# Optimization experiments

Measured on AMD Instinct MI355X. Metric: run time of the kernel, lower is better.

The kernel has to match this reference:

```python
import jax, jax.numpy as jnp
import numpy as np

B, N, D, H, FF = 40, 257, 1024, 16, 4096
HD = D // H
SCALE = HD ** -0.5


def _layernorm(x, w, b, eps=1e-5):
    mu = jnp.mean(x, axis=-1, keepdims=True)
    var = jnp.var(x, axis=-1, keepdims=True)
    return (x - mu) * jax.lax.rsqrt(var + eps) * w + b


def _quick_gelu(x):
    return x * jax.nn.sigmoid(1.702 * x)


def setup_inputs() -> dict:
    key = jax.random.key(0)
    ks = jax.random.split(key, 8)
    s = 0.02
    return {
        'hidden_states': jax.random.normal(ks[0], (B, N, D), jnp.float32),
        'ln1_w': jnp.ones((D,), jnp.float32),
        'ln1_b': jnp.zeros((D,), jnp.float32),
        'wq': jax.random.normal(ks[1], (D, D), jnp.float32) * s,
        'bq': jnp.zeros((D,), jnp.float32),
        'wk': jax.random.normal(ks[2], (D, D), jnp.float32) * s,
        'bk': jnp.zeros((D,), jnp.float32),
        'wv': jax.random.normal(ks[3], (D, D), jnp.float32) * s,
        'bv': jnp.zeros((D,), jnp.float32),
        'wo': jax.random.normal(ks[4], (D, D), jnp.float32) * s,
        'bo': jnp.zeros((D,), jnp.float32),
        'ln2_w': jnp.ones((D,), jnp.float32),
        'ln2_b': jnp.zeros((D,), jnp.float32),
        'fc1_w': jax.random.normal(ks[5], (FF, D), jnp.float32) * s,
        'fc1_b': jnp.zeros((FF,), jnp.float32),
        'fc2_w': jax.random.normal(ks[6], (D, FF), jnp.float32) * s,
        'fc2_b': jnp.zeros((D,), jnp.float32),
    }


def reference(hidden_states, ln1_w, ln1_b, wq, bq, wk, bk, wv, bv, wo, bo,
              ln2_w, ln2_b, fc1_w, fc1_b, fc2_w, fc2_b):
    bsz, n, dim = hidden_states.shape
    residual = hidden_states
    x = _layernorm(hidden_states, ln1_w, ln1_b)
    # QKV projections (torch Linear: y = x @ W^T + b)
    q = (x @ wq.T + bq) * SCALE
    k = x @ wk.T + bk
    v = x @ wv.T + bv
    # [b, h, n, hd]
    q = q.reshape(bsz, n, H, HD).transpose(0, 2, 1, 3)
    k = k.reshape(bsz, n, H, HD).transpose(0, 2, 1, 3)
    v = v.reshape(bsz, n, H, HD).transpose(0, 2, 1, 3)
    scores = jnp.einsum('bhqd,bhkd->bhqk', q, k)  # [b,h,n,n]
    attn = jax.nn.softmax(scores, axis=-1)
    out = jnp.einsum('bhqk,bhkd->bhqd', attn, v)
    out = out.transpose(0, 2, 1, 3).reshape(bsz, n, dim)
    out = out @ wo.T + bo
    hidden = residual + out
    residual = hidden
    h2 = _layernorm(hidden, ln2_w, ln2_b)
    h2 = _quick_gelu(h2 @ fc1_w.T + fc1_b)
    h2 = h2 @ fc2_w.T + fc2_b
    return residual + h2
```

## Files before the change

### kernel.cpp

```cpp
#include <hip/hip_runtime.h>
#include <math.h>

#define D_DIM 1024
#define FF_DIM 4096
#define N_SEQ 257
#define B_SZ 40
#define H_CNT 16
#define HD_DIM 64
#define M_TOK (B_SZ * N_SEQ)
#define VT_NP 320

typedef unsigned short u16;
typedef unsigned char u8;
typedef __bf16 bf16x8 __attribute__((ext_vector_type(8)));
typedef float f32x4 __attribute__((ext_vector_type(4)));
typedef int i32x4 __attribute__((ext_vector_type(4)));

__device__ __forceinline__ float b2f(u16 u) {
    union { unsigned int i; float f; } x; x.i = ((unsigned int)u) << 16; return x.f;
}
__device__ __forceinline__ u16 f2b(float f) {
    union { float f; unsigned int i; } x; x.f = f;
    unsigned int r = x.i + 0x7FFFu + ((x.i >> 16) & 1u);
    return (u16)(r >> 16);
}
__device__ __forceinline__ unsigned q8(float f, float s) {
    int q = __float2int_rn(f * s);
    q = q < -127 ? -127 : (q > 127 ? 127 : q);
    return (unsigned)q & 0xFFu;
}

__device__ __forceinline__ void g2lds16(const void* g, void* l) {
    __builtin_amdgcn_global_load_lds(
        (const __attribute__((address_space(1))) void*)g,
        (__attribute__((address_space(3))) void*)l,
        16, 0, 0);
}

__global__ __launch_bounds__(256)
void cvt_all_kernel(const float* __restrict__ wq, const float* __restrict__ wk,
                    const float* __restrict__ wv, const float* __restrict__ wo,
                    const float* __restrict__ w1, const float* __restrict__ w2,
                    const float* __restrict__ bq, const float* __restrict__ bk,
                    const float* __restrict__ bv,
                    u16* __restrict__ wdst, u8* __restrict__ w1i8,
                    u8* __restrict__ w2i8, float* __restrict__ bqkv) {
    const int nDD = D_DIM * D_DIM, nFD = FF_DIM * D_DIM;
    const int WB8 = (4 * nDD) / 8;
    const int WF8 = (2 * nFD) / 8;
    const int tid = blockIdx.x * 256 + threadIdx.x;
    if (tid < WB8) {
        const int i = tid * 8;
        const float* src; int s;
        if (i < nDD)          { src = wq; s = i; }
        else if (i < 2 * nDD) { src = wk; s = i - nDD; }
        else if (i < 3 * nDD) { src = wv; s = i - 2 * nDD; }
        else                  { src = wo; s = i - 3 * nDD; }
        float4 a = *(const float4*)(src + s);
        float4 b = *(const float4*)(src + s + 4);
        u16 o[8] = {f2b(a.x), f2b(a.y), f2b(a.z), f2b(a.w),
                    f2b(b.x), f2b(b.y), f2b(b.z), f2b(b.w)};
        *(uint4*)(wdst + i) = *(const uint4*)o;
    } else if (tid < WB8 + WF8) {
        const int j = (tid - WB8) * 8;
        const float* src; u8* dst; int s;
        if (j < nFD) { src = w1; dst = w1i8; s = j; }
        else         { src = w2; dst = w2i8; s = j - nFD; }
        float4 a = *(const float4*)(src + s);
        float4 b = *(const float4*)(src + s + 4);
        const float sc = 1024.f;
        unsigned lo = q8(a.x, sc) | (q8(a.y, sc) << 8) |
                      (q8(a.z, sc) << 16) | (q8(a.w, sc) << 24);
        unsigned hi = q8(b.x, sc) | (q8(b.y, sc) << 8) |
                      (q8(b.z, sc) << 16) | (q8(b.w, sc) << 24);
        uint2 pk = {lo, hi};
        *(uint2*)(dst + s) = pk;
    } else {
        const int j = tid - WB8 - WF8;
        if (j < 3 * D_DIM) {
            bqkv[j] = (j < D_DIM) ? bq[j]
                    : (j < 2 * D_DIM ? bk[j - D_DIM] : bv[j - 2 * D_DIM]);
        }
    }
}

template <bool I8OUT>
__global__ __launch_bounds__(256)
void ln_kernel(const float* __restrict__ in, const float* __restrict__ w,
               const float* __restrict__ b, void* __restrict__ out) {
    const int row = blockIdx.x;
    const int t = threadIdx.x;
    const size_t base = (size_t)row * D_DIM;
    float x[4];
#pragma unroll
    for (int i = 0; i < 4; ++i) x[i] = in[base + t + i * 256];
    float s  = x[0] + x[1] + x[2] + x[3];
    float ss = x[0]*x[0] + x[1]*x[1] + x[2]*x[2] + x[3]*x[3];
#pragma unroll
    for (int o = 32; o > 0; o >>= 1) {
        s  += __shfl_xor(s, o, 64);
        ss += __shfl_xor(ss, o, 64);
    }
    __shared__ float sh_s[4], sh_ss[4];
    const int wave = t >> 6, lane = t & 63;
    if (lane == 0) { sh_s[wave] = s; sh_ss[wave] = ss; }
    __syncthreads();
    float S  = sh_s[0] + sh_s[1] + sh_s[2] + sh_s[3];
    float SS = sh_ss[0] + sh_ss[1] + sh_ss[2] + sh_ss[3];
    float mean = S * (1.0f / D_DIM);
    float var  = SS * (1.0f / D_DIM) - mean * mean;
    float rstd = rsqrtf(var + 1e-5f);
#pragma unroll
    for (int i = 0; i < 4; ++i) {
        int idx = t + i * 256;
        float y = (x[i] - mean) * rstd * w[idx] + b[idx];
        if (I8OUT) ((u8*)out)[base + idx]  = (u8)q8(y, 16.f);
        else       ((u16*)out)[base + idx] = f2b(y);
    }
}

#define G256_PHASE(BUF, KH, MH, LOADB, STAGE_STMT)                                   \
  {                                                                                  \
    const u16* sa_ = lds + ((BUF) * 4 + (KH)) * 8192;                                \
    const u16* sb_ = lds + ((BUF) * 4 + 2 + (KH)) * 8192;                            \
    bf16x8 af_[4];                                                                   \
    _Pragma("unroll") for (int mf = 0; mf < 4; ++mf)                                 \
        af_[mf] = *(const bf16x8*)(sa_ + (wr * 128 + (MH) * 64 + mf * 16 + l16) * 32 \
                                       + quad * 8);                                  \
    if (LOADB) {                                                                     \
      _Pragma("unroll") for (int nf = 0; nf < 4; ++nf)                               \
          bf[nf] = *(const bf16x8*)(sb_ + (wc * 64 + nf * 16 + l16) * 32 + quad * 8);\
    }                                                                                \
    asm volatile("s_waitcnt vmcnt(6)" ::: "memory");                                 \
    STAGE_STMT                                                                       \
    asm volatile("" ::: "memory");                                                   \
    __builtin_amdgcn_s_barrier();                                                    \
    asm volatile("" ::: "memory");                                                   \
    __builtin_amdgcn_s_setprio(1);                                                   \
    _Pragma("unroll") for (int mf = 0; mf < 4; ++mf)                                 \
      _Pragma("unroll") for (int nf = 0; nf < 4; ++nf)                               \
          acc[(MH) * 4 + mf][nf] = __builtin_amdgcn_mfma_f32_16x16x32_bf16(          \
              af_[mf], bf[nf], acc[(MH) * 4 + mf][nf], 0, 0, 0);                     \
    __builtin_amdgcn_s_setprio(0);                                                   \
    asm volatile("" ::: "memory");                                                   \
    __builtin_amdgcn_s_barrier();                                                    \
    asm volatile("" ::: "memory");                                                   \
  }

template <int MODE>
__global__ __launch_bounds__(512, 2)
void gemm256_kernel(const u16* __restrict__ A, const u16* __restrict__ Bt,
                    const float* __restrict__ bias, const float* __restrict__ extra,
                    void* __restrict__ out, u16* __restrict__ out2, u16* __restrict__ out3,
                    int M, int N, int K) {
    __shared__ __align__(16) u16 lds[8 * 8192];
    const int t = threadIdx.x;
    const int lane = t & 63, wave = t >> 6;
    const int quad = lane >> 4, l16 = lane & 15;
    const int wr = wave >> 2, wc = wave & 3;

    const int nwg = gridDim.x;
    const int nT = N >> 8;
    const int orig = blockIdx.x;
    const int xcd = orig & 7, loc = orig >> 3;
    const int qq = nwg >> 3, rr = nwg & 7;
    const int wgid = (xcd < rr ? xcd * (qq + 1) : rr * (qq + 1) + (xcd - rr) * qq) + loc;
    const int m0 = (wgid / nT) * 256;
    const int n0 = (wgid % nT) * 256;

    auto stageA = [&](int kt, int kh) {
#pragma unroll
        for (int l = 0; l < 2; ++l) {
            const int c = l * 512 + t;
            int gr = m0 + (c >> 2); if (gr > M - 1) gr = M - 1;
            g2lds16(A + (size_t)gr * K + kt * 64 + kh * 32 + (c & 3) * 8,
                    lds + ((kt & 1) * 4 + kh) * 8192 + c * 8);
        }
    };
    auto stageB = [&](int kt, int kh) {
#pragma unroll
        for (int l = 0; l < 2; ++l) {
            const int c = l * 512 + t;
            g2lds16(Bt + (size_t)(n0 + (c >> 2)) * K + kt * 64 + kh * 32 + (c & 3) * 8,
                    lds + ((kt & 1) * 4 + 2 + kh) * 8192 + c * 8);
        }
    };

    f32x4 acc[8][4];
#pragma unroll
    for (int mi = 0; mi < 8; ++mi)
#pragma unroll
        for (int nf = 0; nf < 4; ++nf) acc[mi][nf] = {0.f, 0.f, 0.f, 0.f};
    bf16x8 bf[4];

    stageA(0, 0); stageB(0, 0); stageA(0, 1); stageB(0, 1); stageA(1, 0); stageB(1, 0);
    asm volatile("s_waitcnt vmcnt(0)" ::: "memory");
    __builtin_amdgcn_s_barrier();
    asm volatile("" ::: "memory");

    const int NIT = K >> 7;
    for (int i = 0; i < NIT; ++i) {
        const int kt0 = 2 * i;
        const bool more = (i < NIT - 1);
        G256_PHASE(0, 0, 0, true,  { stageA(kt0 + 1, 1); })
        G256_PHASE(0, 0, 1, false, { stageB(kt0 + 1, 1); })
        G256_PHASE(0, 1, 0, true,  { if (more) stageA(kt0 + 2, 0); })
        G256_PHASE(0, 1, 1, false, { if (more) stageB(kt0 + 2, 0); })
        G256_PHASE(1, 0, 0, true,  { if (more) stageA(kt0 + 2, 1); })
        G256_PHASE(1, 0, 1, false, { if (more) stageB(kt0 + 2, 1); })
        G256_PHASE(1, 1, 0, true,  { if (more) stageA(kt0 + 3, 0); })
        G256_PHASE(1, 1, 1, false, { if (more) stageB(kt0 + 3, 0); })
    }

#pragma unroll
    for (int mi = 0; mi < 8; ++mi) {
#pragma unroll
        for (int nf = 0; nf < 4; ++nf) {
            const int n = n0 + wc * 64 + nf * 16 + l16;
            const float bvf = bias[n];
#pragma unroll
            for (int i2 = 0; i2 < 4; ++i2) {
                const int m = m0 + wr * 128 + mi * 16 + quad * 4 + i2;
                if (m >= M) continue;
                float v = acc[mi][nf][i2] + bvf;
                if (MODE == 2) {
                    const size_t idx = (size_t)m * N + n;
                    ((float*)out)[idx] = extra[idx] + v;
                } else {
                    const int seg = n >> 10, nl = n & 1023;
                    if (seg == 0) {
                        ((u16*)out)[(size_t)m * D_DIM + nl] = f2b(v * 0.125f);
                    } else if (seg == 1) {
                        out2[(size_t)m * D_DIM + nl] = f2b(v);
                    } else {
                        const int bb = m / N_SEQ;
                        const int tt = m - bb * N_SEQ;
                        out3[((size_t)bb * D_DIM + nl) * VT_NP + tt] = f2b(v);
                    }
                }
            }
        }
    }
}

template <int MODE>
__global__ __launch_bounds__(256)
void gemm_i8_kernel(const u8* __restrict__ A, const u8* __restrict__ Bt,
                    const float* __restrict__ bias, const float* __restrict__ extra,
                    void* __restrict__ out, int M, int N, int K, int sw) {
    __shared__ __align__(16) u8 sA[128 * 128];
    __shared__ __align__(16) u8 sB[128 * 128];
    const int t = threadIdx.x;

    const int nM = gridDim.x, nN = gridDim.y;
    const int lid   = blockIdx.y * nM + blockIdx.x;
    const int csz   = sw * nN;
    const int chunk = lid / csz;
    const int rem   = lid - chunk * csz;
    const int n0 = (rem % nN) * 128;
    const int m0 = (chunk * sw + rem / nN) * 128;

    const int wave = t >> 6, lane = t & 63;
    const int quad = lane >> 4, l16 = lane & 15;
    const int wm = (wave >> 1) * 64, wn = (wave & 1) * 64;

    const u8* gA[4]; const u8* gB[4]; u8* lA[4]; u8* lB[4];
#pragma unroll
    for (int i = 0; i < 4; ++i) {
        const int c = i * 256 + t;
        const int row = c >> 3;
        const int sg = (c & 7) ^ (row & 7);
        int gr = m0 + row; if (gr > M - 1) gr = M - 1;
        gA[i] = A  + (size_t)gr * K + sg * 16;
        gB[i] = Bt + (size_t)(n0 + row) * K + sg * 16;
        lA[i] = sA + c * 16;
        lB[i] = sB + c * 16;
    }

    i32x4 acc[4][4];
#pragma unroll
    for (int mt = 0; mt < 4; ++mt)
#pragma unroll
        for (int nt = 0; nt < 4; ++nt) acc[mt][nt] = {0, 0, 0, 0};

    for (int k0 = 0; k0 < K; k0 += 128) {
        __syncthreads();
#pragma unroll
        for (int i = 0; i < 4; ++i) g2lds16(gA[i] + k0, lA[i]);
#pragma unroll
        for (int i = 0; i < 4; ++i) g2lds16(gB[i] + k0, lB[i]);
        __syncthreads();
#pragma unroll
        for (int j = 0; j < 2; ++j) {
            i32x4 af[4], bfr[4];
#pragma unroll
            for (int mt = 0; mt < 4; ++mt) {
                const int r = wm + mt * 16 + l16;
                af[mt] = *(const i32x4*)(sA + r * 128 + (((j * 4 + quad) ^ (r & 7)) * 16));
            }
#pragma unroll
            for (int nt = 0; nt < 4; ++nt) {
                const int n = wn + nt * 16 + l16;
                bfr[nt] = *(const i32x4*)(sB + n * 128 + (((j * 4 + quad) ^ (n & 7)) * 16));
            }
#pragma unroll
            for (int mt = 0; mt < 4; ++mt)
#pragma unroll
                for (int nt = 0; nt < 4; ++nt)
                    acc[mt][nt] = __builtin_amdgcn_mfma_i32_16x16x64_i8(
                        af[mt], bfr[nt], acc[mt][nt], 0, 0, 0);
        }
    }

    const float sc = (MODE == 2) ? (1.f / 32768.f) : (1.f / 16384.f);
#pragma unroll
    for (int mt = 0; mt < 4; ++mt) {
#pragma unroll
        for (int nt = 0; nt < 4; ++nt) {
            const int n = n0 + wn + nt * 16 + l16;
            const float bvf = bias[n];
#pragma unroll
            for (int i = 0; i < 4; ++i) {
                const int m = m0 + wm + mt * 16 + quad * 4 + i;
                if (m >= M) continue;
                float v = (float)acc[mt][nt][i] * sc + bvf;
                if (MODE == 2) {
                    const size_t idx = (size_t)m * N + n;
                    ((float*)out)[idx] = extra[idx] + v;
                } else {
                    float g = v / (1.0f + __expf(-1.702f * v));
                    ((u8*)out)[(size_t)m * N + n] = (u8)q8(g, 32.f);
                }
            }
        }
    }
}

#define ATT_PS 296
__global__ __launch_bounds__(256, 4)
void attn_mfma_kernel(const u16* __restrict__ q, const u16* __restrict__ k,
                      const u16* __restrict__ vT, u16* __restrict__ o) {
    __shared__ __align__(16) u16 sP[64 * ATT_PS];
    __shared__ float sInv[64];

    const int t = threadIdx.x;
    const int wave = t >> 6, lane = t & 63;
    const int quad = lane >> 4, l16 = lane & 15;

    const int lid = blockIdx.x;
    const int g = lid / 40, local = lid - g * 40;
    const int qt = local >> 3, x = local & 7;
    const int hb = g * 8 + x;
    const int h = hb & (H_CNT - 1), b = hb >> 4;
    const int q0 = qt * 64;
    const size_t head = (size_t)b * N_SEQ * D_DIM + (size_t)h * HD_DIM;

    int qrow = q0 + wave * 16 + l16; if (qrow > N_SEQ - 1) qrow = N_SEQ - 1;
    const u16* qp = q + head + (size_t)qrow * D_DIM + quad * 8;
    bf16x8 qf0 = *(const bf16x8*)(qp);
    bf16x8 qf1 = *(const bf16x8*)(qp + 32);

    f32x4 s[5][4];
#pragma unroll
    for (int kt = 0; kt < 5; ++kt) {
        const int ntMax = (kt == 4) ? 2 : 4;
#pragma unroll
        for (int nt = 0; nt < 4; ++nt) {
            if (nt >= ntMax) continue;
            s[kt][nt] = {0.f, 0.f, 0.f, 0.f};
            int key = kt * 64 + nt * 16 + l16;
            if (key > N_SEQ - 1) key = N_SEQ - 1;
            const u16* kr = k + head + (size_t)key * D_DIM + quad * 8;
            bf16x8 b0 = *(const bf16x8*)(kr);
            bf16x8 b1 = *(const bf16x8*)(kr + 32);
            s[kt][nt] = __builtin_amdgcn_mfma_f32_16x16x32_bf16(qf0, b0, s[kt][nt], 0, 0, 0);
            s[kt][nt] = __builtin_amdgcn_mfma_f32_16x16x32_bf16(qf1, b1, s[kt][nt], 0, 0, 0);
        }
    }

#pragma unroll
    for (int i = 0; i < 4; ++i) {
        float mx = -1e30f;
#pragma unroll
        for (int kt = 0; kt < 5; ++kt) {
            const int ntMax = (kt == 4) ? 2 : 4;
#pragma unroll
            for (int nt = 0; nt < 4; ++nt) {
                if (nt >= ntMax) continue;
                const bool valid = (kt < 4) || (nt == 0 && l16 == 0);
                if (valid) mx = fmaxf(mx, s[kt][nt][i]);
            }
        }
        mx = fmaxf(mx, __shfl_xor(mx, 1, 64));
        mx = fmaxf(mx, __shfl_xor(mx, 2, 64));
        mx = fmaxf(mx, __shfl_xor(mx, 4, 64));
        mx = fmaxf(mx, __shfl_xor(mx, 8, 64));
        float sum = 0.f;
        const int prow = wave * 16 + quad * 4 + i;
#pragma unroll
        for (int kt = 0; kt < 5; ++kt) {
            const int ntMax = (kt == 4) ? 2 : 4;
#pragma unroll
            for (int nt = 0; nt < 4; ++nt) {
                if (nt >= ntMax) continue;
                const bool valid = (kt < 4) || (nt == 0 && l16 == 0);
                float pv = 0.f;
                if (valid) { pv = __expf(s[kt][nt][i] - mx); sum += pv; }
                sP[prow * ATT_PS + kt * 64 + nt * 16 + l16] = f2b(pv);
            }
        }
        sum += __shfl_xor(sum, 1, 64);
        sum += __shfl_xor(sum, 2, 64);
        sum += __shfl_xor(sum, 4, 64);
        sum += __shfl_xor(sum, 8, 64);
        if (l16 == 0) sInv[prow] = 1.0f / sum;
    }
    __syncthreads();

    f32x4 oacc[4] = {{0.f,0.f,0.f,0.f},{0.f,0.f,0.f,0.f},
                     {0.f,0.f,0.f,0.f},{0.f,0.f,0.f,0.f}};
    const u16* vhead = vT + ((size_t)b * D_DIM + h * HD_DIM) * VT_NP;
    const int prr = wave * 16 + l16;
#pragma unroll
    for (int kt = 0; kt < 5; ++kt) {
        const int j0 = kt * 64;
        bf16x8 p0 = *(const bf16x8*)(sP + prr * ATT_PS + j0 + quad * 8);
        bf16x8 p1;
        if (kt < 4) p1 = *(const bf16x8*)(sP + prr * ATT_PS + j0 + quad * 8 + 32);
#pragma unroll
        for (int nt = 0; nt < 4; ++nt) {
            const u16* vr = vhead + (size_t)(nt * 16 + l16) * VT_NP + j0 + quad * 8;
            bf16x8 b0 = *(const bf16x8*)(vr);
            oacc[nt] = __builtin_amdgcn_mfma_f32_16x16x32_bf16(p0, b0, oacc[nt], 0, 0, 0);
            if (kt < 4) {
                bf16x8 b1 = *(const bf16x8*)(vr + 32);
                oacc[nt] = __builtin_amdgcn_mfma_f32_16x16x32_bf16(p1, b1, oacc[nt], 0, 0, 0);
            }
        }
    }
#pragma unroll
    for (int nt = 0; nt < 4; ++nt) {
#pragma unroll
        for (int i = 0; i < 4; ++i) {
            const int mrow = wave * 16 + quad * 4 + i;
            const int m = q0 + mrow;
            if (m < N_SEQ) {
                o[head + (size_t)m * D_DIM + nt * 16 + l16] =
                    f2b(oacc[nt][i] * sInv[mrow]);
            }
        }
    }
}

extern "C" void kernel_launch(void* const* d_in, const int* in_sizes, int n_in,
                              void* d_out, int out_size, void* d_ws, size_t ws_size,
                              hipStream_t stream) {
    const float* hs   = (const float*)d_in[0];
    const float* ln1w = (const float*)d_in[1];
    const float* ln1b = (const float*)d_in[2];
    const float* wq   = (const float*)d_in[3];
    const float* bq   = (const float*)d_in[4];
    const float* wk   = (const float*)d_in[5];
    const float* bk   = (const float*)d_in[6];
    const float* wv   = (const float*)d_in[7];
    const float* bv   = (const float*)d_in[8];
    const float* wo   = (const float*)d_in[9];
    const float* bo   = (const float*)d_in[10];
    const float* ln2w = (const float*)d_in[11];
    const float* ln2b = (const float*)d_in[12];
    const float* w1   = (const float*)d_in[13];
    const float* b1   = (const float*)d_in[14];
    const float* w2   = (const float*)d_in[15];
    const float* b2   = (const float*)d_in[16];

    char* p = (char*)d_ws;
    size_t off = 0;
    auto alloc = [&](size_t bytes) {
        char* r = p + off;
        off += (bytes + 255) & ~(size_t)255;
        return (void*)r;
    };
    const int M = M_TOK;
    u16* wqkvb = (u16*)alloc((size_t)3 * D_DIM * D_DIM * 2);
    u16* wob   = (u16*)alloc((size_t)D_DIM * D_DIM * 2);
    u8*  w1i8  = (u8*) alloc((size_t)FF_DIM * D_DIM);
    u8*  w2i8  = (u8*) alloc((size_t)D_DIM * FF_DIM);
    float* bqkv = (float*)alloc((size_t)3 * D_DIM * 4);
    u16*  x_ln = (u16*) alloc((size_t)M * D_DIM * 2);
    u16*  qb   = (u16*) alloc((size_t)M * D_DIM * 2);
    u16*  kb   = (u16*) alloc((size_t)M * D_DIM * 2);
    u16*  vTb  = (u16*) alloc((size_t)B_SZ * D_DIM * VT_NP * 2);
    u16*  ab   = (u16*) alloc((size_t)M * D_DIM * 2);
    float* hid = (float*)alloc((size_t)M * D_DIM * 4);
    u8* h1i8 = (u8*)qb;
    u8* x2i8 = (u8*)ab;

    const int nDD = D_DIM * D_DIM, nFD = FF_DIM * D_DIM;
    const int WB8 = (4 * nDD) / 8, WF8 = (2 * nFD) / 8;
    cvt_all_kernel<<<(WB8 + WF8 + 3 * D_DIM + 255) / 256, 256, 0, stream>>>(
        wq, wk, wv, wo, w1, w2, bq, bk, bv, wqkvb, w1i8, w2i8, bqkv);

    ln_kernel<false><<<M, 256, 0, stream>>>(hs, ln1w, ln1b, x_ln);

    const int gM256 = (M + 255) / 256;
    gemm256_kernel<5><<<gM256 * (3 * D_DIM / 256), 512, 0, stream>>>(
        x_ln, wqkvb, bqkv, nullptr, qb, kb, vTb, M, 3 * D_DIM, D_DIM);

    attn_mfma_kernel<<<5 * H_CNT * B_SZ, 256, 0, stream>>>(qb, kb, vTb, ab);

    gemm256_kernel<2><<<gM256 * (D_DIM / 256), 512, 0, stream>>>(
        ab, wob, bo, hs, hid, nullptr, nullptr, M, D_DIM, D_DIM);

    ln_kernel<true><<<M, 256, 0, stream>>>(hid, ln2w, ln2b, x2i8);

    const int gM = (M + 127) / 128;
    dim3 gF(gM, FF_DIM / 128);
    gemm_i8_kernel<3><<<gF, 256, 0, stream>>>(x2i8, w1i8, b1, nullptr, h1i8,
                                              M, FF_DIM, D_DIM, 16);
    dim3 gD(gM, D_DIM / 128);
    gemm_i8_kernel<2><<<gD, 256, 0, stream>>>(h1i8, w2i8, b2, hid, (float*)d_out,
                                              M, D_DIM, FF_DIM, 4);
}
```

Before: 611.6 us.

## Restructure bf16 GEMM k-loop into four phases with XOR-swizzled LDS layout

The 256x256 bf16 GEMM main loop is collapsed from eight half-phases into four. Each phase loads A and B fragments, issues the A and B stage for a future k-slice, and runs both M-halves of MFMAs, with one barrier per phase instead of two. LDS rows are XOR-swizzled on both the global-to-LDS staging and the fragment reads to cut bank conflicts. The vmcnt waits are relaxed to keep more loads in flight. The risk is a tighter dependency between in-flight loads and buffer reuse, plus more register pressure from holding separate B fragments per phase.

Result: no change. 609.7 us (-0.3%).

```diff
diff --git a/kernel.cpp b/kernel.cpp
--- a/kernel.cpp
+++ b/kernel.cpp
@@ -119,30 +119,29 @@
     }
 }
 
-#define G256_PHASE(BUF, KH, MH, LOADB, STAGE_STMT)                                   \
+#define G256_PHASE(BUF, KH, KT_S, KH_S, DOSTAGE)                                     \
   {                                                                                  \
     const u16* sa_ = lds + ((BUF) * 4 + (KH)) * 8192;                                \
     const u16* sb_ = lds + ((BUF) * 4 + 2 + (KH)) * 8192;                            \
-    bf16x8 af_[4];                                                                   \
+    bf16x8 af[4], bfv[4];                                                            \
     _Pragma("unroll") for (int mf = 0; mf < 4; ++mf)                                 \
-        af_[mf] = *(const bf16x8*)(sa_ + (wr * 128 + (MH) * 64 + mf * 16 + l16) * 32 \
-                                       + quad * 8);                                  \
-    if (LOADB) {                                                                     \
-      _Pragma("unroll") for (int nf = 0; nf < 4; ++nf)                               \
-          bf[nf] = *(const bf16x8*)(sb_ + (wc * 64 + nf * 16 + l16) * 32 + quad * 8);\
-    }                                                                                \
-    asm volatile("s_waitcnt vmcnt(6)" ::: "memory");                                 \
-    STAGE_STMT                                                                       \
-    asm volatile("" ::: "memory");                                                   \
-    __builtin_amdgcn_s_barrier();                                                    \
-    asm volatile("" ::: "memory");                                                   \
+        af[mf] = *(const bf16x8*)(sa_ + (wr * 128 + mf * 16 + l16) * 32 + xch);      \
+    _Pragma("unroll") for (int nf = 0; nf < 4; ++nf)                                 \
+        bfv[nf] = *(const bf16x8*)(sb_ + (wc * 64 + nf * 16 + l16) * 32 + xch);      \
+    if (DOSTAGE) { stageA(KT_S, KH_S); stageB(KT_S, KH_S); }                         \
     __builtin_amdgcn_s_setprio(1);                                                   \
     _Pragma("unroll") for (int mf = 0; mf < 4; ++mf)                                 \
       _Pragma("unroll") for (int nf = 0; nf < 4; ++nf)                               \
-          acc[(MH) * 4 + mf][nf] = __builtin_amdgcn_mfma_f32_16x16x32_bf16(          \
-              af_[mf], bf[nf], acc[(MH) * 4 + mf][nf], 0, 0, 0);                     \
+          acc[mf][nf] = __builtin_amdgcn_mfma_f32_16x16x32_bf16(                     \
+              af[mf], bfv[nf], acc[mf][nf], 0, 0, 0);                                \
+    _Pragma("unroll") for (int mf = 0; mf < 4; ++mf)                                 \
+        af[mf] = *(const bf16x8*)(sa_ + (wr * 128 + 64 + mf * 16 + l16) * 32 + xch); \
+    _Pragma("unroll") for (int mf = 0; mf < 4; ++mf)                                 \
+      _Pragma("unroll") for (int nf = 0; nf < 4; ++nf)                               \
+          acc[4 + mf][nf] = __builtin_amdgcn_mfma_f32_16x16x32_bf16(                 \
+              af[mf], bfv[nf], acc[4 + mf][nf], 0, 0, 0);                            \
     __builtin_amdgcn_s_setprio(0);                                                   \
-    asm volatile("" ::: "memory");                                                   \
+    asm volatile("s_waitcnt vmcnt(8)" ::: "memory");                                 \
     __builtin_amdgcn_s_barrier();                                                    \
     asm volatile("" ::: "memory");                                                   \
   }
@@ -158,6 +157,7 @@
     const int lane = t & 63, wave = t >> 6;
     const int quad = lane >> 4, l16 = lane & 15;
     const int wr = wave >> 2, wc = wave & 3;
+    const int xch = (quad ^ ((l16 >> 1) & 3)) * 8;
 
     const int nwg = gridDim.x;
     const int nT = N >> 8;
@@ -173,7 +173,8 @@
         for (int l = 0; l < 2; ++l) {
             const int c = l * 512 + t;
             int gr = m0 + (c >> 2); if (gr > M - 1) gr = M - 1;
-            g2lds16(A + (size_t)gr * K + kt * 64 + kh * 32 + (c & 3) * 8,
+            const int sg = (c & 3) ^ ((c >> 3) & 3);
+            g2lds16(A + (size_t)gr * K + kt * 64 + kh * 32 + sg * 8,
                     lds + ((kt & 1) * 4 + kh) * 8192 + c * 8);
         }
     };
@@ -181,7 +182,8 @@
 #pragma unroll
         for (int l = 0; l < 2; ++l) {
             const int c = l * 512 + t;
-            g2lds16(Bt + (size_t)(n0 + (c >> 2)) * K + kt * 64 + kh * 32 + (c & 3) * 8,
+            const int sg = (c & 3) ^ ((c >> 3) & 3);
+            g2lds16(Bt + (size_t)(n0 + (c >> 2)) * K + kt * 64 + kh * 32 + sg * 8,
                     lds + ((kt & 1) * 4 + 2 + kh) * 8192 + c * 8);
         }
     };
@@ -191,10 +193,9 @@
     for (int mi = 0; mi < 8; ++mi)
 #pragma unroll
         for (int nf = 0; nf < 4; ++nf) acc[mi][nf] = {0.f, 0.f, 0.f, 0.f};
-    bf16x8 bf[4];
 
     stageA(0, 0); stageB(0, 0); stageA(0, 1); stageB(0, 1); stageA(1, 0); stageB(1, 0);
-    asm volatile("s_waitcnt vmcnt(0)" ::: "memory");
+    asm volatile("s_waitcnt vmcnt(8)" ::: "memory");
     __builtin_amdgcn_s_barrier();
     asm volatile("" ::: "memory");
 
@@ -202,14 +203,10 @@
     for (int i = 0; i < NIT; ++i) {
         const int kt0 = 2 * i;
         const bool more = (i < NIT - 1);
-        G256_PHASE(0, 0, 0, true,  { stageA(kt0 + 1, 1); })
-        G256_PHASE(0, 0, 1, false, { stageB(kt0 + 1, 1); })
-        G256_PHASE(0, 1, 0, true,  { if (more) stageA(kt0 + 2, 0); })
-        G256_PHASE(0, 1, 1, false, { if (more) stageB(kt0 + 2, 0); })
-        G256_PHASE(1, 0, 0, true,  { if (more) stageA(kt0 + 2, 1); })
-        G256_PHASE(1, 0, 1, false, { if (more) stageB(kt0 + 2, 1); })
-        G256_PHASE(1, 1, 0, true,  { if (more) stageA(kt0 + 3, 0); })
-        G256_PHASE(1, 1, 1, false, { if (more) stageB(kt0 + 3, 0); })
+        G256_PHASE(0, 0, kt0 + 1, 1, true)
+        G256_PHASE(0, 1, kt0 + 2, 0, more)
+        G256_PHASE(1, 0, kt0 + 2, 1, more)
+        G256_PHASE(1, 1, kt0 + 3, 0, more)
     }
 
 #pragma unroll
@@ -321,7 +318,7 @@
             const float bvf = bias[n];
 #pragma unroll
             for (int i = 0; i < 4; ++i) {
-                const int m = m0 + wm + mt * 16 + quad * 4 + i;
+                const int m = m0 + wm + quad * 4 + i + mt * 16;
                 if (m >= M) continue;
                 float v = (float)acc[mt][nt][i] * sc + bvf;
                 if (MODE == 2) {
```
